# Kernel optimization log

Hardware: AMD Instinct MI355X
Metric: run time of the kernel (lower is better)

## Reference

```python
import jax, jax.numpy as jnp
import numpy as np

N, IN_F, HID, HEADS, OUT_F, E, G = 20000, 256, 128, 4, 10, 400000, 64
HC = HID * HEADS  # 512


def gatv2_layer(x, src, dst, Wl, bl, Wr, br, att, bias, num_nodes):
    # PyG GATv2Conv (concat=True): lin_l for source msgs, lin_r for targets
    H, C = att.shape
    xl = (x @ Wl + bl).reshape(-1, H, C)
    xr = (x @ Wr + br).reshape(-1, H, C)
    # edge-wise GATv2 score: a^T LeakyReLU(xl_j + xr_i)
    e = jax.nn.leaky_relu(xl[src] + xr[dst], 0.2)          # [E,H,C]
    logits = jnp.einsum('ehc,hc->eh', e, att)              # [E,H]
    # segment softmax over incoming edges of each destination node
    m = jax.ops.segment_max(logits, dst, num_segments=num_nodes)
    p = jnp.exp(logits - m[dst])
    denom = jax.ops.segment_sum(p, dst, num_segments=num_nodes)
    alpha = p / denom[dst]                                 # [E,H]
    out = jax.ops.segment_sum(alpha[:, :, None] * xl[src], dst,
                              num_segments=num_nodes)      # [N,H,C]
    return out.reshape(num_nodes, H * C) + bias


def setup_inputs() -> dict:
    key = jax.random.key(0)
    ks = jax.random.split(key, 32)
    s = 0.05
    inp = {
        'x': jax.random.normal(ks[0], (N, IN_F), jnp.float32),
        'edge_index': jax.random.randint(ks[1], (2, E), 0, N, jnp.int64),
        'batch': jnp.sort(jax.random.randint(ks[2], (N,), 0, G, jnp.int64)),
        'pre_W': jax.random.normal(ks[3], (IN_F, HID), jnp.float32) * s,
        'pre_b': jnp.zeros((HID,), jnp.float32),
        'cls_W': jax.random.normal(ks[4], (HC, OUT_F), jnp.float32) * s,
        'cls_b': jnp.zeros((OUT_F,), jnp.float32),
    }
    in_dims = [HID, HC, HC]
    for i in range(3):
        kk = jax.random.split(ks[5 + i], 6)
        d = in_dims[i]
        inp[f'Wl{i+1}'] = jax.random.normal(kk[0], (d, HC), jnp.float32) * s
        inp[f'bl{i+1}'] = jnp.zeros((HC,), jnp.float32)
        inp[f'Wr{i+1}'] = jax.random.normal(kk[1], (d, HC), jnp.float32) * s
        inp[f'br{i+1}'] = jnp.zeros((HC,), jnp.float32)
        inp[f'att{i+1}'] = jax.random.normal(kk[2], (HEADS, HID), jnp.float32) * s
        inp[f'bias{i+1}'] = jnp.zeros((HC,), jnp.float32)
    return inp


def reference(x, edge_index, batch, pre_W, pre_b, cls_W, cls_b,
              Wl1, bl1, Wr1, br1, att1, bias1,
              Wl2, bl2, Wr2, br2, att2, bias2,
              Wl3, bl3, Wr3, br3, att3, bias3):
    num_nodes = x.shape[0]
    # add self loops (PyG GATv2Conv default)
    loop = jnp.arange(num_nodes, dtype=edge_index.dtype)
    src = jnp.concatenate([edge_index[0], loop])
    dst = jnp.concatenate([edge_index[1], loop])

    h = jax.nn.elu(x @ pre_W + pre_b)  # dropout is identity in eval
    h = jax.nn.elu(gatv2_layer(h, src, dst, Wl1, bl1, Wr1, br1, att1, bias1, num_nodes))
    h = jax.nn.elu(gatv2_layer(h, src, dst, Wl2, bl2, Wr2, br2, att2, bias2, num_nodes))
    h = jax.nn.elu(gatv2_layer(h, src, dst, Wl3, bl3, Wr3, br3, att3, bias3, num_nodes))
    # global mean pool over graphs
    sums = jax.ops.segment_sum(h, batch, num_segments=G)
    cnts = jax.ops.segment_sum(jnp.ones((num_nodes,), h.dtype), batch, num_segments=G)
    pooled = sums / jnp.maximum(cnts, 1.0)[:, None]
    return pooled @ cls_W + cls_b
```

## Files before the change

kernel.cpp:

```cpp
#include <hip/hip_runtime.h>
#include <hip/hip_bf16.h>
#include <math.h>

#define NODES   20000
#define MPAD    20096
#define IN_F    256
#define HID     128
#define HEADS   4
#define OUT_F   10
#define NEDGE   400000
#define NGRAPH  64
#define HC      512
#define EPRIME  (NEDGE + NODES)
#define XLRW    1024

typedef __attribute__((ext_vector_type(8))) short bf16x8_t;
typedef __attribute__((ext_vector_type(4))) float f32x4_t;

__device__ __forceinline__ unsigned short bf16_rne(float f) {
    unsigned int u = __float_as_uint(f);
    u += 0x7FFFu + ((u >> 16) & 1u);
    return (unsigned short)(u >> 16);
}
__device__ __forceinline__ float bf16f(unsigned short h) {
    return __uint_as_float(((unsigned int)h) << 16);
}
__device__ __forceinline__ void split2(float f, unsigned short& hi, unsigned short& lo) {
    hi = bf16_rne(f);
    lo = bf16_rne(f - bf16f(hi));
}

#define GLOAD_LDS16(gp, lp) \
    __builtin_amdgcn_global_load_lds((const __attribute__((address_space(1))) unsigned int*)(gp), \
                                     (__attribute__((address_space(3))) unsigned int*)(lp), 16, 0, 0)

__global__ __launch_bounds__(256) void hist_kernel(const int* __restrict__ ei,
                                                   int* __restrict__ counts) {
    int e = blockIdx.x * blockDim.x + threadIdx.x;
    if (e >= EPRIME) return;
    int dst = (e < NEDGE) ? ei[NEDGE + e] : (e - NEDGE);
    atomicAdd(&counts[dst], 1);
}

__global__ __launch_bounds__(1024) void scan_kernel(const int* __restrict__ counts,
                                                    int* __restrict__ offsets,
                                                    int* __restrict__ cursor) {
    __shared__ int wsum[16];
    __shared__ int s_carry;
    const int tid = threadIdx.x;
    const int lane = tid & 63, wid = tid >> 6;
    if (tid == 0) s_carry = 0;
    __syncthreads();
    for (int base = 0; base < NODES; base += 1024) {
        int idx = base + tid;
        int v = (idx < NODES) ? counts[idx] : 0;
        int x = v;
        #pragma unroll
        for (int d = 1; d < 64; d <<= 1) {
            int n = __shfl_up(x, d);
            if (lane >= d) x += n;
        }
        if (lane == 63) wsum[wid] = x;
        __syncthreads();
        if (wid == 0) {
            int w = (lane < 16) ? wsum[lane] : 0;
            #pragma unroll
            for (int d = 1; d < 16; d <<= 1) {
                int n = __shfl_up(w, d);
                if (lane >= d) w += n;
            }
            if (lane < 16) wsum[lane] = w;
        }
        __syncthreads();
        int carry = s_carry;
        int wpre = (wid == 0) ? 0 : wsum[wid - 1];
        int excl = carry + wpre + x - v;
        if (idx < NODES) { offsets[idx] = excl; cursor[idx] = excl; }
        __syncthreads();
        if (tid == 1023) s_carry = carry + wsum[15];
        __syncthreads();
    }
    if (tid == 0) offsets[NODES] = s_carry;
}

__global__ __launch_bounds__(256) void scatter_kernel(const int* __restrict__ ei,
                                                      int* __restrict__ cursor,
                                                      int* __restrict__ srcsb) {
    int e = blockIdx.x * blockDim.x + threadIdx.x;
    if (e >= EPRIME) return;
    int src, dst;
    if (e < NEDGE) { src = ei[e]; dst = ei[NEDGE + e]; }
    else           { src = dst = e - NEDGE; }
    int pos = atomicAdd(&cursor[dst], 1);
    srcsb[pos] = src << 12;
}

__global__ __launch_bounds__(256) void convert_x_kernel(const float* __restrict__ x,
                                                        unsigned short* __restrict__ x2) {
    int idx = blockIdx.x * 256 + threadIdx.x;
    int r = idx >> 5, g = idx & 31;
    if (r >= MPAD) return;
    __align__(16) unsigned short hv[8], lv[8];
    if (r < NODES) {
        const float* p = &x[(size_t)r * IN_F + g * 8];
        #pragma unroll
        for (int j = 0; j < 8; ++j) split2(p[j], hv[j], lv[j]);
    } else {
        #pragma unroll
        for (int j = 0; j < 8; ++j) { hv[j] = 0; lv[j] = 0; }
    }
    unsigned short* o = x2 + (size_t)r * (2 * IN_F) + g * 16;
    *reinterpret_cast<uint4*>(o)     = *reinterpret_cast<uint4*>(hv);
    *reinterpret_cast<uint4*>(o + 8) = *reinterpret_cast<uint4*>(lv);
}

__global__ __launch_bounds__(256) void convert_w_kernel(const float* __restrict__ W,
                                                        unsigned short* __restrict__ WT2,
                                                        int K, int N, int gshift) {
    int idx = blockIdx.x * 256 + threadIdx.x;
    int n = idx >> gshift, g = idx & ((1 << gshift) - 1);
    if (n >= N) return;
    __align__(16) unsigned short hv[8], lv[8];
    #pragma unroll
    for (int j = 0; j < 8; ++j) split2(W[(size_t)(8 * g + j) * N + n], hv[j], lv[j]);
    unsigned short* o = WT2 + (size_t)n * (2 * K) + g * 16;
    *reinterpret_cast<uint4*>(o)     = *reinterpret_cast<uint4*>(hv);
    *reinterpret_cast<uint4*>(o + 8) = *reinterpret_cast<uint4*>(lv);
}

__global__ __launch_bounds__(256) void build_bias_kernel(const float* __restrict__ bl1,
                                                         const float* __restrict__ br1,
                                                         const float* __restrict__ bl2,
                                                         const float* __restrict__ br2,
                                                         const float* __restrict__ bl3,
                                                         const float* __restrict__ br3,
                                                         float* __restrict__ out) {
    int idx = blockIdx.x * 256 + threadIdx.x;
    if (idx >= 3 * 1024) return;
    int l = idx >> 10, c = idx & 1023;
    const float* p = (l == 0) ? (c < 512 ? bl1 : br1)
                   : (l == 1) ? (c < 512 ? bl2 : br2)
                              : (c < 512 ? bl3 : br3);
    out[idx] = p[c & 511];
}

template <int WRITE_SPLIT, int ACT>
__global__ __launch_bounds__(256) void mfma_gemm_kernel(const unsigned short* __restrict__ A2,
                                                        const unsigned short* __restrict__ B2,
                                                        const float* __restrict__ bias,
                                                        float* __restrict__ Cf,
                                                        unsigned short* __restrict__ C2,
                                                        int M, int N, int K) {
    __shared__ char lds[32768];
    const int tid = threadIdx.x;
    const int w = tid >> 6, l = tid & 63;
    const int wr = w >> 1, wc = w & 1;
    const int row0 = blockIdx.x * 128, col0 = blockIdx.y * 128;
    const size_t rowB = (size_t)K * 4;

    f32x4_t acc[4][4];
    #pragma unroll
    for (int i = 0; i < 4; ++i)
        #pragma unroll
        for (int j = 0; j < 4; ++j)
            #pragma unroll
            for (int q = 0; q < 4; ++q) acc[i][j][q] = 0.f;

    const int ssub = l >> 3;
    const int scol = (l & 7) * 16;
    const int g16  = l >> 4;
    const int fr   = l & 15;

    const char* Ab = (const char*)A2;
    const char* Bb = (const char*)B2;

    const int nsteps = K >> 5;
    for (int t = 0; t < nsteps; ++t) {
        #pragma unroll
        for (int i = 0; i < 4; ++i) {
            int r = w * 32 + i * 8 + ssub;
            size_t gb = (size_t)(row0 + r) * rowB + (size_t)t * 128 + (size_t)(scol ^ ((r & 7) << 4));
            GLOAD_LDS16(Ab + gb, &lds[(w * 32 + i * 8) * 128]);
        }
        #pragma unroll
        for (int i = 0; i < 4; ++i) {
            int r = w * 32 + i * 8 + ssub;
            size_t gb = (size_t)(col0 + r) * rowB + (size_t)t * 128 + (size_t)(scol ^ ((r & 7) << 4));
            GLOAD_LDS16(Bb + gb, &lds[16384 + (w * 32 + i * 8) * 128]);
        }
        asm volatile("s_waitcnt vmcnt(0)" ::: "memory");
        __syncthreads();

        bf16x8_t ah[4], al[4];
        #pragma unroll
        for (int i = 0; i < 4; ++i) {
            int r = wr * 64 + i * 16 + fr;
            int sw = (r & 7) << 4;
            ah[i] = *reinterpret_cast<const bf16x8_t*>(&lds[r * 128 + ((g16 * 32) ^ sw)]);
            al[i] = *reinterpret_cast<const bf16x8_t*>(&lds[r * 128 + ((g16 * 32 + 16) ^ sw)]);
        }
        #pragma unroll
        for (int j = 0; j < 4; ++j) {
            int r = wc * 64 + j * 16 + fr;
            int sw = (r & 7) << 4;
            bf16x8_t bh = *reinterpret_cast<const bf16x8_t*>(&lds[16384 + r * 128 + ((g16 * 32) ^ sw)]);
            bf16x8_t bl = *reinterpret_cast<const bf16x8_t*>(&lds[16384 + r * 128 + ((g16 * 32 + 16) ^ sw)]);
            #pragma unroll
            for (int i = 0; i < 4; ++i) {
                acc[i][j] = __builtin_amdgcn_mfma_f32_16x16x32_bf16(ah[i], bh, acc[i][j], 0, 0, 0);
                acc[i][j] = __builtin_amdgcn_mfma_f32_16x16x32_bf16(ah[i], bl, acc[i][j], 0, 0, 0);
                acc[i][j] = __builtin_amdgcn_mfma_f32_16x16x32_bf16(al[i], bh, acc[i][j], 0, 0, 0);
            }
        }
        __syncthreads();
    }

    const int crb  = (l >> 4) * 4;
    const int ccol = l & 15;
    #pragma unroll
    for (int i = 0; i < 4; ++i) {
        #pragma unroll
        for (int jj = 0; jj < 4; ++jj) {
            int rg = row0 + wr * 64 + i * 16 + crb + jj;
            #pragma unroll
            for (int j = 0; j < 4; ++j) {
                int cg = col0 + wc * 64 + j * 16 + ccol;
                float v = acc[i][j][jj] + bias[cg];
                if (ACT) v = v > 0.f ? v : expm1f(v);
                if (WRITE_SPLIT) {
                    unsigned short hi, lo;
                    split2(v, hi, lo);
                    unsigned short* o = C2 + (size_t)rg * (2 * N) + (cg >> 3) * 16 + (cg & 7);
                    o[0] = hi; o[8] = lo;
                } else {
                    if (rg < M) Cf[(size_t)rg * N + cg] = v;
                }
            }
        }
    }
}

__global__ __launch_bounds__(256) void gat_edge_kernel(const float* __restrict__ xlr,
                                                       const float* __restrict__ att,
                                                       const float* __restrict__ bias,
                                                       const int* __restrict__ offsets,
                                                       const int* __restrict__ srcsb,
                                                       unsigned short* __restrict__ h2) {
    const int node = blockIdx.x;
    if (node >= NODES) {
        uint2* o = (uint2*)(h2 + (size_t)node * (2 * HC));
        o[threadIdx.x] = make_uint2(0u, 0u);
        return;
    }
    const int h = threadIdx.x >> 6, lane = threadIdx.x & 63;
    const int c0 = lane * 2;
    const int ch = h * HID + c0;
    const char* xlb = (const char*)xlr;
    const int laneoff = ch * 4;
    const float2 xrv = *reinterpret_cast<const float2*>(&xlr[(size_t)node * XLRW + 512 + ch]);
    float2 atv = *reinterpret_cast<const float2*>(&att[ch]);
    atv.x *= 1.44269504f; atv.y *= 1.44269504f;
    const int beg = offsets[node], end = offsets[node + 1];

    float m = -INFINITY, denom = 0.f, a0 = 0.f, a1 = 0.f;
    const bool b5 = (lane & 32) != 0, b4 = (lane & 16) != 0;

    for (int e0 = beg; e0 < end; e0 += 4) {
        const int nb = min(4, end - e0);
        int sb[4]; float2 xv[4]; float p[4];
        #pragma unroll
        for (int q = 0; q < 4; ++q) sb[q] = srcsb[e0 + ((q < nb) ? q : nb - 1)];
        #pragma unroll
        for (int q = 0; q < 4; ++q)
            xv[q] = *reinterpret_cast<const float2*>(xlb + (size_t)(unsigned)sb[q] + laneoff);
        #pragma unroll
        for (int q = 0; q < 4; ++q) {
            float v0 = xv[q].x + xrv.x; v0 = fmaxf(v0, 0.2f * v0);
            float v1 = xv[q].y + xrv.y; v1 = fmaxf(v1, 0.2f * v1);
            p[q] = fmaf(atv.y, v1, atv.x * v0);
        }
        float s0 = b5 ? p[0] : p[2];
        float u0 = (b5 ? p[2] : p[0]) + __shfl_xor(s0, 32);
        float s1 = b5 ? p[1] : p[3];
        float u1 = (b5 ? p[3] : p[1]) + __shfl_xor(s1, 32);
        float s2 = b4 ? u0 : u1;
        float t  = (b4 ? u1 : u0) + __shfl_xor(s2, 16);
        t += __shfl_xor(t, 8);
        t += __shfl_xor(t, 4);
        t += __shfl_xor(t, 2);
        t += __shfl_xor(t, 1);
        const float pe0 = __shfl(t, 0);
        const float pe1 = __shfl(t, 16);
        const float pe2 = __shfl(t, 32);
        const float pe3 = __shfl(t, 48);

        const float m4 = fmaxf(fmaxf(pe0, pe1), fmaxf(pe2, pe3));
        if (m4 > m) {
            float sc = exp2f(m - m4);
            denom *= sc; a0 *= sc; a1 *= sc; m = m4;
        }
        {
            float w0 = exp2f(pe0 - m);
            denom += w0; a0 = fmaf(w0, xv[0].x, a0); a1 = fmaf(w0, xv[0].y, a1);
        }
        if (nb > 1) {
            float w1 = exp2f(pe1 - m);
            denom += w1; a0 = fmaf(w1, xv[1].x, a0); a1 = fmaf(w1, xv[1].y, a1);
        }
        if (nb > 2) {
            float w2 = exp2f(pe2 - m);
            denom += w2; a0 = fmaf(w2, xv[2].x, a0); a1 = fmaf(w2, xv[2].y, a1);
        }
        if (nb > 3) {
            float w3 = exp2f(pe3 - m);
            denom += w3; a0 = fmaf(w3, xv[3].x, a0); a1 = fmaf(w3, xv[3].y, a1);
        }
    }

    const float inv = 1.f / denom;
    const float2 bv = *reinterpret_cast<const float2*>(&bias[ch]);
    float o0 = a0 * inv + bv.x, o1 = a1 * inv + bv.y;
    o0 = o0 > 0.f ? o0 : expm1f(o0);
    o1 = o1 > 0.f ? o1 : expm1f(o1);
    unsigned short h0, l0, h1, l1;
    split2(o0, h0, l0); split2(o1, h1, l1);
    unsigned short* o = h2 + (size_t)node * (2 * HC) + (ch >> 3) * 16 + (ch & 7);
    o[0] = h0; o[1] = h1; o[8] = l0; o[9] = l1;
}

__global__ __launch_bounds__(256) void pool_part_kernel(const unsigned short* __restrict__ h2,
                                                        const int* __restrict__ batch,
                                                        float* __restrict__ partial) {
    const int g = blockIdx.x, part = blockIdx.y;
    int lo = 0, hi = NODES;
    while (lo < hi) { int mid = (lo + hi) >> 1; if (batch[mid] < g) lo = mid + 1; else hi = mid; }
    const int s = lo;
    lo = s; hi = NODES;
    while (lo < hi) { int mid = (lo + hi) >> 1; if (batch[mid] < g + 1) lo = mid + 1; else hi = mid; }
    const int e = lo, cnt = e - s;
    const int ps = s + (cnt * part) / 4;
    const int pe = s + (cnt * (part + 1)) / 4;

    const int c0 = threadIdx.x * 2;
    const int boff = ((c0 >> 3) * 16) + (c0 & 7);
    float s0 = 0.f, s1 = 0.f;
    for (int r = ps; r < pe; ++r) {
        const unsigned short* p = h2 + (size_t)r * (2 * HC) + boff;
        s0 += bf16f(p[0]) + bf16f(p[8]);
        s1 += bf16f(p[1]) + bf16f(p[9]);
    }
    float* o = partial + ((size_t)(g * 4 + part)) * HC;
    o[c0] = s0; o[c0 + 1] = s1;
}

__global__ __launch_bounds__(256) void cls_kernel(const float* __restrict__ partial,
                                                  const int* __restrict__ batch,
                                                  const float* __restrict__ W,
                                                  const float* __restrict__ cb,
                                                  float* __restrict__ outp) {
    const int g = blockIdx.x;
    __shared__ float pooled[HC];
    int lo = 0, hi = NODES;
    while (lo < hi) { int mid = (lo + hi) >> 1; if (batch[mid] < g) lo = mid + 1; else hi = mid; }
    const int s = lo;
    lo = s; hi = NODES;
    while (lo < hi) { int mid = (lo + hi) >> 1; if (batch[mid] < g + 1) lo = mid + 1; else hi = mid; }
    const int cnt = lo - s;

    const int c0 = threadIdx.x * 2;
    float s0 = 0.f, s1 = 0.f;
    #pragma unroll
    for (int part = 0; part < 4; ++part) {
        const float* p = partial + ((size_t)(g * 4 + part)) * HC;
        s0 += p[c0]; s1 += p[c0 + 1];
    }
    const float invc = cnt > 0 ? 1.f / (float)cnt : 0.f;
    pooled[c0] = s0 * invc; pooled[c0 + 1] = s1 * invc;
    __syncthreads();

    const int lane = threadIdx.x & 63, wid = threadIdx.x >> 6;
    for (int o = wid; o < OUT_F; o += 4) {
        float p = 0.f;
        for (int c = lane; c < HC; c += 64) p += pooled[c] * W[c * OUT_F + o];
        #pragma unroll
        for (int off2 = 32; off2; off2 >>= 1) p += __shfl_xor(p, off2);
        if (lane == 0) outp[g * OUT_F + o] = p + cb[o];
    }
}

extern "C" void kernel_launch(void* const* d_in, const int* in_sizes, int n_in,
                              void* d_out, int out_size, void* d_ws, size_t ws_size,
                              hipStream_t stream) {
    const float* x      = (const float*)d_in[0];
    const int*   ei     = (const int*)d_in[1];
    const int*   batch  = (const int*)d_in[2];
    const float* pre_W  = (const float*)d_in[3];
    const float* pre_b  = (const float*)d_in[4];
    const float* cls_W  = (const float*)d_in[5];
    const float* cls_b  = (const float*)d_in[6];
    const float* Wl[3]; const float* bl[3]; const float* Wr[3];
    const float* br[3]; const float* attw[3]; const float* bw[3];
    for (int l = 0; l < 3; ++l) {
        Wl[l]   = (const float*)d_in[7 + 6 * l + 0];
        bl[l]   = (const float*)d_in[7 + 6 * l + 1];
        Wr[l]   = (const float*)d_in[7 + 6 * l + 2];
        br[l]   = (const float*)d_in[7 + 6 * l + 3];
        attw[l] = (const float*)d_in[7 + 6 * l + 4];
        bw[l]   = (const float*)d_in[7 + 6 * l + 5];
    }
    float* outp = (float*)d_out;

    char* ws = (char*)d_ws;
    size_t off = 0;
    auto alloc = [&](size_t b) { char* p = ws + off; off += (b + 255) & ~(size_t)255; return p; };
    float* xlr = (float*)alloc((size_t)MPAD * XLRW * 4);
    unsigned short* h2 = (unsigned short*)alloc((size_t)MPAD * 2 * HC * 2);
    unsigned short* WT2f = (unsigned short*)alloc((size_t)1024 * 2 * HC * 2);
    unsigned short* preWT2 = (unsigned short*)alloc((size_t)HID * 2 * IN_F * 2);
    float* biascat = (float*)alloc(3 * 1024 * 4);
    int* counts  = (int*)alloc(NODES * 4);
    int* offsets = (int*)alloc((NODES + 1) * 4);
    int* cursor  = (int*)alloc(NODES * 4);
    int* srcsb   = (int*)alloc((size_t)EPRIME * 4);
    unsigned short* x2 = (unsigned short*)xlr;
    float* partial = xlr;

    hipMemsetAsync(counts, 0, NODES * 4, stream);
    hist_kernel<<<(EPRIME + 255) / 256, 256, 0, stream>>>(ei, counts);
    scan_kernel<<<1, 1024, 0, stream>>>(counts, offsets, cursor);
    scatter_kernel<<<(EPRIME + 255) / 256, 256, 0, stream>>>(ei, cursor, srcsb);

    convert_x_kernel<<<(MPAD * (IN_F / 8) + 255) / 256, 256, 0, stream>>>(x, x2);
    convert_w_kernel<<<(HID * (IN_F / 8) + 255) / 256, 256, 0, stream>>>(pre_W, preWT2, IN_F, HID, 5);
    build_bias_kernel<<<12, 256, 0, stream>>>(bl[0], br[0], bl[1], br[1], bl[2], br[2], biascat);
    convert_w_kernel<<<(HC * (HID / 8) + 255) / 256, 256, 0, stream>>>(Wl[0], WT2f, HID, HC, 4);
    convert_w_kernel<<<(HC * (HID / 8) + 255) / 256, 256, 0, stream>>>(Wr[0], WT2f + (size_t)512 * 2 * HID, HID, HC, 4);

    mfma_gemm_kernel<1, 1><<<dim3(157, 1), 256, 0, stream>>>(x2, preWT2, pre_b,
                                                             nullptr, h2, NODES, HID, IN_F);

    mfma_gemm_kernel<0, 0><<<dim3(157, 8), 256, 0, stream>>>(h2, WT2f, biascat, xlr, nullptr, NODES, 1024, HID);
    convert_w_kernel<<<(HC * (HC / 8) + 255) / 256, 256, 0, stream>>>(Wl[1], WT2f, HC, HC, 6);
    convert_w_kernel<<<(HC * (HC / 8) + 255) / 256, 256, 0, stream>>>(Wr[1], WT2f + (size_t)512 * 2 * HC, HC, HC, 6);
    gat_edge_kernel<<<MPAD, 256, 0, stream>>>(xlr, attw[0], bw[0], offsets, srcsb, h2);

    mfma_gemm_kernel<0, 0><<<dim3(157, 8), 256, 0, stream>>>(h2, WT2f, biascat + 1024, xlr, nullptr, NODES, 1024, HC);
    convert_w_kernel<<<(HC * (HC / 8) + 255) / 256, 256, 0, stream>>>(Wl[2], WT2f, HC, HC, 6);
    convert_w_kernel<<<(HC * (HC / 8) + 255) / 256, 256, 0, stream>>>(Wr[2], WT2f + (size_t)512 * 2 * HC, HC, HC, 6);
    gat_edge_kernel<<<MPAD, 256, 0, stream>>>(xlr, attw[1], bw[1], offsets, srcsb, h2);

    mfma_gemm_kernel<0, 0><<<dim3(157, 8), 256, 0, stream>>>(h2, WT2f, biascat + 2048, xlr, nullptr, NODES, 1024, HC);
    gat_edge_kernel<<<MPAD, 256, 0, stream>>>(xlr, attw[2], bw[2], offsets, srcsb, h2);

    pool_part_kernel<<<dim3(NGRAPH, 4), 256, 0, stream>>>(h2, batch, partial);
    cls_kernel<<<NGRAPH, 256, 0, stream>>>(partial, batch, cls_W, cls_b, outp);
}
```

Measured before the change: 826.1 us.

## Process four channels per thread in GATv2 edge kernel with packed FP32 math

The edge aggregation kernel now uses 128 threads per node instead of 256. Each thread handles four channels with float4 gathers, so 32 lanes cover a head. LeakyReLU is rewritten as 0.6*x + 0.4*|x| so the attention dot product can use packed v_pk_add/mul/fma instructions, and the per-edge score broadcast uses ds_bpermute with a reduction tree adjusted to the new lane mapping. The aim is fewer instructions per edge and wider memory transactions. The cost is more registers per thread and half the threads per block to hide gather latency.

```diff
diff --git a/kernel.cpp b/kernel.cpp
--- a/kernel.cpp
+++ b/kernel.cpp
@@ -16,6 +16,28 @@
 
 typedef __attribute__((ext_vector_type(8))) short bf16x8_t;
 typedef __attribute__((ext_vector_type(4))) float f32x4_t;
+
+__device__ __forceinline__ float2 pk_add(float2 a, float2 b) {
+    float2 d;
+    asm("v_pk_add_f32 %0, %1, %2" : "=v"(d) : "v"(a), "v"(b));
+    return d;
+}
+__device__ __forceinline__ float2 pk_mul(float2 a, float2 b) {
+    float2 d;
+    asm("v_pk_mul_f32 %0, %1, %2" : "=v"(d) : "v"(a), "v"(b));
+    return d;
+}
+__device__ __forceinline__ float2 pk_fma(float2 a, float2 b, float2 c) {
+    float2 d;
+    asm("v_pk_fma_f32 %0, %1, %2, %3" : "=v"(d) : "v"(a), "v"(b), "v"(c));
+    return d;
+}
+__device__ __forceinline__ float2 abs2(float2 s) {
+    float2 r;
+    r.x = __uint_as_float(__float_as_uint(s.x) & 0x7fffffffu);
+    r.y = __uint_as_float(__float_as_uint(s.y) & 0x7fffffffu);
+    return r;
+}
 
 __device__ __forceinline__ unsigned short bf16_rne(float f) {
     unsigned int u = __float_as_uint(f);
@@ -240,7 +262,7 @@
     }
 }
 
-__global__ __launch_bounds__(256) void gat_edge_kernel(const float* __restrict__ xlr,
+__global__ __launch_bounds__(128) void gat_edge_kernel(const float* __restrict__ xlr,
                                                        const float* __restrict__ att,
                                                        const float* __restrict__ bias,
                                                        const int* __restrict__ offsets,
@@ -248,84 +270,116 @@
                                                        unsigned short* __restrict__ h2) {
     const int node = blockIdx.x;
     if (node >= NODES) {
-        uint2* o = (uint2*)(h2 + (size_t)node * (2 * HC));
-        o[threadIdx.x] = make_uint2(0u, 0u);
+        ((uint4*)(h2 + (size_t)node * (2 * HC)))[threadIdx.x] = make_uint4(0u, 0u, 0u, 0u);
         return;
     }
-    const int h = threadIdx.x >> 6, lane = threadIdx.x & 63;
-    const int c0 = lane * 2;
-    const int ch = h * HID + c0;
+    const int tid = threadIdx.x;
+    const int head = tid >> 5;
+    const int hl   = tid & 31;
+    const int wl   = tid & 63;
+    const int ch0  = head * HID + hl * 4;
     const char* xlb = (const char*)xlr;
-    const int laneoff = ch * 4;
-    const float2 xrv = *reinterpret_cast<const float2*>(&xlr[(size_t)node * XLRW + 512 + ch]);
-    float2 atv = *reinterpret_cast<const float2*>(&att[ch]);
-    atv.x *= 1.44269504f; atv.y *= 1.44269504f;
+    const int laneoff = ch0 * 4;
+
+    const float4 atv = *reinterpret_cast<const float4*>(&att[ch0]);
+    const float L2E = 1.44269504f;
+    const float2 a6p0 = make_float2(0.6f * L2E * atv.x, 0.6f * L2E * atv.y);
+    const float2 a6p1 = make_float2(0.6f * L2E * atv.z, 0.6f * L2E * atv.w);
+    const float2 a4p0 = make_float2(0.4f * L2E * atv.x, 0.4f * L2E * atv.y);
+    const float2 a4p1 = make_float2(0.4f * L2E * atv.z, 0.4f * L2E * atv.w);
+    const float4 xrv = *reinterpret_cast<const float4*>(&xlr[(size_t)node * XLRW + 512 + ch0]);
+    const float2 xrp0 = make_float2(xrv.x, xrv.y);
+    const float2 xrp1 = make_float2(xrv.z, xrv.w);
+
+    const int ibase = ((wl & 32) + (wl & 7)) << 2;
+    const int idx0 = ibase, idx1 = ibase + (8 << 2);
+    const int idx2 = ibase + (16 << 2), idx3 = ibase + (24 << 2);
+
     const int beg = offsets[node], end = offsets[node + 1];
-
-    float m = -INFINITY, denom = 0.f, a0 = 0.f, a1 = 0.f;
-    const bool b5 = (lane & 32) != 0, b4 = (lane & 16) != 0;
+    const bool b4 = (hl & 16) != 0, b3 = (hl & 8) != 0;
+
+    float m = -INFINITY, denom = 0.f;
+    float a0 = 0.f, a1 = 0.f, a2 = 0.f, a3 = 0.f;
 
     for (int e0 = beg; e0 < end; e0 += 4) {
         const int nb = min(4, end - e0);
-        int sb[4]; float2 xv[4]; float p[4];
+        int sb[4]; float4 xv[4]; float p[4];
         #pragma unroll
         for (int q = 0; q < 4; ++q) sb[q] = srcsb[e0 + ((q < nb) ? q : nb - 1)];
         #pragma unroll
         for (int q = 0; q < 4; ++q)
-            xv[q] = *reinterpret_cast<const float2*>(xlb + (size_t)(unsigned)sb[q] + laneoff);
+            xv[q] = *reinterpret_cast<const float4*>(xlb + (size_t)(unsigned)sb[q] + laneoff);
         #pragma unroll
         for (int q = 0; q < 4; ++q) {
-            float v0 = xv[q].x + xrv.x; v0 = fmaxf(v0, 0.2f * v0);
-            float v1 = xv[q].y + xrv.y; v1 = fmaxf(v1, 0.2f * v1);
-            p[q] = fmaf(atv.y, v1, atv.x * v0);
-        }
-        float s0 = b5 ? p[0] : p[2];
-        float u0 = (b5 ? p[2] : p[0]) + __shfl_xor(s0, 32);
-        float s1 = b5 ? p[1] : p[3];
-        float u1 = (b5 ? p[3] : p[1]) + __shfl_xor(s1, 32);
-        float s2 = b4 ? u0 : u1;
-        float t  = (b4 ? u1 : u0) + __shfl_xor(s2, 16);
-        t += __shfl_xor(t, 8);
+            float2 s0 = pk_add(make_float2(xv[q].x, xv[q].y), xrp0);
+            float2 s1 = pk_add(make_float2(xv[q].z, xv[q].w), xrp1);
+            float2 pp = pk_mul(a6p0, s0);
+            pp = pk_fma(a4p0, abs2(s0), pp);
+            pp = pk_fma(a6p1, s1, pp);
+            pp = pk_fma(a4p1, abs2(s1), pp);
+            p[q] = pp.x + pp.y;
+        }
+        float s0 = b4 ? p[0] : p[2];
+        float u0 = (b4 ? p[2] : p[0]) + __shfl_xor(s0, 16);
+        float s1 = b4 ? p[1] : p[3];
+        float u1 = (b4 ? p[3] : p[1]) + __shfl_xor(s1, 16);
+        float s2 = b3 ? u0 : u1;
+        float t  = (b3 ? u1 : u0) + __shfl_xor(s2, 8);
         t += __shfl_xor(t, 4);
         t += __shfl_xor(t, 2);
         t += __shfl_xor(t, 1);
-        const float pe0 = __shfl(t, 0);
-        const float pe1 = __shfl(t, 16);
-        const float pe2 = __shfl(t, 32);
-        const float pe3 = __shfl(t, 48);
+        const int ti = __float_as_int(t);
+        const float pe0 = __int_as_float(__builtin_amdgcn_ds_bpermute(idx0, ti));
+        const float pe1 = __int_as_float(__builtin_amdgcn_ds_bpermute(idx1, ti));
+        const float pe2 = __int_as_float(__builtin_amdgcn_ds_bpermute(idx2, ti));
+        const float pe3 = __int_as_float(__builtin_amdgcn_ds_bpermute(idx3, ti));
 
         const float m4 = fmaxf(fmaxf(pe0, pe1), fmaxf(pe2, pe3));
         if (m4 > m) {
             float sc = exp2f(m - m4);
-            denom *= sc; a0 *= sc; a1 *= sc; m = m4;
+            denom *= sc; a0 *= sc; a1 *= sc; a2 *= sc; a3 *= sc;
+            m = m4;
         }
         {
             float w0 = exp2f(pe0 - m);
-            denom += w0; a0 = fmaf(w0, xv[0].x, a0); a1 = fmaf(w0, xv[0].y, a1);
+            denom += w0;
+            a0 = fmaf(w0, xv[0].x, a0); a1 = fmaf(w0, xv[0].y, a1);
+            a2 = fmaf(w0, xv[0].z, a2); a3 = fmaf(w0, xv[0].w, a3);
         }
         if (nb > 1) {
             float w1 = exp2f(pe1 - m);
-            denom += w1; a0 = fmaf(w1, xv[1].x, a0); a1 = fmaf(w1, xv[1].y, a1);
+            denom += w1;
+            a0 = fmaf(w1, xv[1].x, a0); a1 = fmaf(w1, xv[1].y, a1);
+            a2 = fmaf(w1, xv[1].z, a2); a3 = fmaf(w1, xv[1].w, a3);
         }
         if (nb > 2) {
             float w2 = exp2f(pe2 - m);
-            denom += w2; a0 = fmaf(w2, xv[2].x, a0); a1 = fmaf(w2, xv[2].y, a1);
+            denom += w2;
+            a0 = fmaf(w2, xv[2].x, a0); a1 = fmaf(w2, xv[2].y, a1);
+            a2 = fmaf(w2, xv[2].z, a2); a3 = fmaf(w2, xv[2].w, a3);
         }
         if (nb > 3) {
             float w3 = exp2f(pe3 - m);
-            denom += w3; a0 = fmaf(w3, xv[3].x, a0); a1 = fmaf(w3, xv[3].y, a1);
+            denom += w3;
+            a0 = fmaf(w3, xv[3].x, a0); a1 = fmaf(w3, xv[3].y, a1);
+            a2 = fmaf(w3, xv[3].z, a2); a3 = fmaf(w3, xv[3].w, a3);
         }
     }
 
     const float inv = 1.f / denom;
-    const float2 bv = *reinterpret_cast<const float2*>(&bias[ch]);
+    const float4 bv = *reinterpret_cast<const float4*>(&bias[ch0]);
     float o0 = a0 * inv + bv.x, o1 = a1 * inv + bv.y;
+    float o2 = a2 * inv + bv.z, o3 = a3 * inv + bv.w;
     o0 = o0 > 0.f ? o0 : expm1f(o0);
     o1 = o1 > 0.f ? o1 : expm1f(o1);
-    unsigned short h0, l0, h1, l1;
-    split2(o0, h0, l0); split2(o1, h1, l1);
-    unsigned short* o = h2 + (size_t)node * (2 * HC) + (ch >> 3) * 16 + (ch & 7);
-    o[0] = h0; o[1] = h1; o[8] = l0; o[9] = l1;
+    o2 = o2 > 0.f ? o2 : expm1f(o2);
+    o3 = o3 > 0.f ? o3 : expm1f(o3);
+    __align__(8) unsigned short hv[4], lv[4];
+    split2(o0, hv[0], lv[0]); split2(o1, hv[1], lv[1]);
+    split2(o2, hv[2], lv[2]); split2(o3, hv[3], lv[3]);
+    unsigned short* o = h2 + (size_t)node * (2 * HC) + ((ch0 >> 3) * 16) + (ch0 & 7);
+    *reinterpret_cast<uint2*>(o)     = *reinterpret_cast<uint2*>(hv);
+    *reinterpret_cast<uint2*>(o + 8) = *reinterpret_cast<uint2*>(lv);
 }
 
 __global__ __launch_bounds__(256) void pool_part_kernel(const unsigned short* __restrict__ h2,
@@ -442,15 +496,15 @@
     mfma_gemm_kernel<0, 0><<<dim3(157, 8), 256, 0, stream>>>(h2, WT2f, biascat, xlr, nullptr, NODES, 1024, HID);
     convert_w_kernel<<<(HC * (HC / 8) + 255) / 256, 256, 0, stream>>>(Wl[1], WT2f, HC, HC, 6);
     convert_w_kernel<<<(HC * (HC / 8) + 255) / 256, 256, 0, stream>>>(Wr[1], WT2f + (size_t)512 * 2 * HC, HC, HC, 6);
-    gat_edge_kernel<<<MPAD, 256, 0, stream>>>(xlr, attw[0], bw[0], offsets, srcsb, h2);
+    gat_edge_kernel<<<MPAD, 128, 0, stream>>>(xlr, attw[0], bw[0], offsets, srcsb, h2);
 
     mfma_gemm_kernel<0, 0><<<dim3(157, 8), 256, 0, stream>>>(h2, WT2f, biascat + 1024, xlr, nullptr, NODES, 1024, HC);
     convert_w_kernel<<<(HC * (HC / 8) + 255) / 256, 256, 0, stream>>>(Wl[2], WT2f, HC, HC, 6);
     convert_w_kernel<<<(HC * (HC / 8) + 255) / 256, 256, 0, stream>>>(Wr[2], WT2f + (size_t)512 * 2 * HC, HC, HC, 6);
-    gat_edge_kernel<<<MPAD, 256, 0, stream>>>(xlr, attw[1], bw[1], offsets, srcsb, h2);
+    gat_edge_kernel<<<MPAD, 128, 0, stream>>>(xlr, attw[1], bw[1], offsets, srcsb, h2);
 
     mfma_gemm_kernel<0, 0><<<dim3(157, 8), 256, 0, stream>>>(h2, WT2f, biascat + 2048, xlr, nullptr, NODES, 1024, HC);
-    gat_edge_kernel<<<MPAD, 256, 0, stream>>>(xlr, attw[2], bw[2], offsets, srcsb, h2);
+    gat_edge_kernel<<<MPAD, 128, 0, stream>>>(xlr, attw[2], bw[2], offsets, srcsb, h2);
 
     pool_part_kernel<<<dim3(NGRAPH, 4), 256, 0, stream>>>(h2, batch, partial);
     cls_kernel<<<NGRAPH, 256, 0, stream>>>(partial, batch, cls_W, cls_b, outp);
```

Result: no change. 830.9 us (+0.6%).
